# Performance work log

Measured on AMD Instinct MI355X. Metric: run time of the kernel, lower is better.

## Reference

```python
import jax, jax.numpy as jnp
import numpy as np

D_MODEL = 1024
NHEAD = 16
D_K = D_MODEL // NHEAD
THETA_NC = 0.01
B, S = 2, 2048

def setup_inputs() -> dict:
    key = jax.random.key(0)
    ks = jax.random.split(key, 8)
    lim = 1.0 / np.sqrt(D_MODEL)
    return {
        "x": jax.random.normal(ks[0], (B, S, D_MODEL), dtype=jnp.float32),
        "Wq": jax.random.uniform(ks[1], (D_MODEL, D_MODEL), jnp.float32, -lim, lim),
        "Wk": jax.random.uniform(ks[2], (D_MODEL, D_MODEL), jnp.float32, -lim, lim),
        "Wv": jax.random.uniform(ks[3], (D_MODEL, D_MODEL), jnp.float32, -lim, lim),
        "Wo": jax.random.uniform(ks[4], (D_MODEL, D_MODEL), jnp.float32, -lim, lim),
        "bo": jnp.zeros((D_MODEL,), jnp.float32),
        "gauge_phase": jnp.zeros((NHEAD,), jnp.float32),
        "gauge_amplitude": jnp.ones((NHEAD,), jnp.float32),
        "nc_mixing": jax.random.normal(ks[5], (NHEAD, D_K, D_K), jnp.float32) * THETA_NC,
    }

def reference(x, Wq, Wk, Wv, Wo, bo, gauge_phase, gauge_amplitude, nc_mixing):
    b, s, _ = x.shape
    # QKV projections (torch Linear: x @ W.T), reshape to [b, h, s, d_k]
    def proj(W):
        return (x @ W.T).reshape(b, s, NHEAD, D_K).transpose(0, 2, 1, 3)
    Q, K, V = proj(Wq), proj(Wk), proj(Wv)
    # gauge: real part of exp(i*phase) is cos(phase); amplitude scale per head
    g = (gauge_amplitude * jnp.cos(gauge_phase)).reshape(1, NHEAD, 1, 1)
    Q_nc = jnp.einsum('bhnd,hdk->bhnk', Q * g, nc_mixing)
    K_nc = jnp.einsum('bhnd,hdk->bhnk', K * g, nc_mixing)
    scores = jnp.einsum('bhnk,bhmk->bhnm', Q_nc, K_nc) / jnp.sqrt(jnp.float32(D_K))
    attn = jax.nn.softmax(scores, axis=-1)
    ctx = jnp.einsum('bhnm,bhmd->bhnd', attn, V)
    ctx = ctx.transpose(0, 2, 1, 3).reshape(b, s, D_MODEL)
    out = ctx @ Wo.T + bo
    return out, attn
```

## Files before the change

### kernel.cpp

```cpp
#include <hip/hip_runtime.h>

typedef short bf16x8 __attribute__((ext_vector_type(8)));
typedef float f32x4 __attribute__((ext_vector_type(4)));
typedef unsigned short u16;

__device__ __forceinline__ u16 f2bf(float f) {
  union { float f; unsigned u; } v; v.f = f;
  unsigned r = v.u + 0x7fffu + ((v.u >> 16) & 1u);
  return (u16)(r >> 16);
}
__device__ __forceinline__ float bf2f(u16 s) {
  union { unsigned u; float f; } v; v.u = ((unsigned)s) << 16;
  return v.f;
}

__global__ __launch_bounds__(256) void fold_kernel(
    const float* __restrict__ Wq, const float* __restrict__ Wk,
    const float* __restrict__ phase, const float* __restrict__ amp,
    const float* __restrict__ nc,
    u16* __restrict__ WqE, u16* __restrict__ WkE) {
  __shared__ float ncS[64 * 64];
  __shared__ float WS[64 * 65];
  int bid = blockIdx.x;
  int sel = bid >> 8, h = (bid >> 4) & 15, d0 = (bid & 15) * 64;
  const float* W = sel ? Wk : Wq;
  u16* O = sel ? WkE : WqE;
  float g = amp[h] * cosf(phase[h]);
  float sc = g * (sel ? 1.0f : 0.125f * 1.44269504088896f);
  int t = threadIdx.x;
  for (int l = t; l < 4096; l += 256) ncS[l] = nc[h * 4096 + l];
  for (int l = t; l < 4096; l += 256) {
    int e = l >> 6, dd = l & 63;
    WS[e * 65 + dd] = W[(h * 64 + e) * 1024 + d0 + dd];
  }
  __syncthreads();
  int kp = t >> 2, q = t & 3;
  for (int dd = q * 16; dd < q * 16 + 16; ++dd) {
    float acc = 0.f;
#pragma unroll
    for (int e = 0; e < 64; ++e) acc += WS[e * 65 + dd] * ncS[e * 64 + kp];
    O[(h * 64 + kp) * 1024 + d0 + dd] = f2bf(acc * sc);
  }
}

__global__ __launch_bounds__(256) void cast_kernel(const float* __restrict__ src,
                                                   u16* __restrict__ dst, int n4) {
  int i = blockIdx.x * 256 + threadIdx.x;
  if (i >= n4) return;
  float4 v = ((const float4*)src)[i];
  ushort4 o;
  o.x = f2bf(v.x); o.y = f2bf(v.y); o.z = f2bf(v.z); o.w = f2bf(v.w);
  ((ushort4*)dst)[i] = o;
}

__global__ __launch_bounds__(256) void split_kernel(const float* __restrict__ src,
                                                    u16* __restrict__ hi, u16* __restrict__ lo, int n4) {
  int i = blockIdx.x * 256 + threadIdx.x;
  if (i >= n4) return;
  float4 v = ((const float4*)src)[i];
  ushort4 h, l;
  h.x = f2bf(v.x); l.x = f2bf(v.x - bf2f(h.x));
  h.y = f2bf(v.y); l.y = f2bf(v.y - bf2f(h.y));
  h.z = f2bf(v.z); l.z = f2bf(v.z - bf2f(h.z));
  h.w = f2bf(v.w); l.w = f2bf(v.w - bf2f(h.w));
  ((ushort4*)hi)[i] = h;
  ((ushort4*)lo)[i] = l;
}

#define LDA 72
__global__ __launch_bounds__(256) void proj_gemm(
    const u16* __restrict__ A, const u16* __restrict__ W0, const u16* __restrict__ W1,
    const u16* __restrict__ W2, u16* __restrict__ Qnc, u16* __restrict__ Knc,
    u16* __restrict__ Vt) {
  __shared__ u16 As[128 * LDA];
  __shared__ u16 Bs[128 * LDA];
  int z = blockIdx.z;
  const u16* Wp = (z == 0) ? W0 : ((z == 1) ? W1 : W2);
  int m0 = blockIdx.x * 128, n0 = blockIdx.y * 128;
  int t = threadIdx.x, lane = t & 63, wid = t >> 6;
  int wr = wid >> 1, wc = wid & 1;
  f32x4 acc[4][4] = {};
  for (int k0 = 0; k0 < 1024; k0 += 64) {
    __syncthreads();
#pragma unroll
    for (int it = 0; it < 4; ++it) {
      int q = it * 256 + t;
      int row = q >> 3, c8 = (q & 7) * 8;
      *(bf16x8*)&As[row * LDA + c8] = *(const bf16x8*)&A[(m0 + row) * 1024 + k0 + c8];
      *(bf16x8*)&Bs[row * LDA + c8] = *(const bf16x8*)&Wp[(n0 + row) * 1024 + k0 + c8];
    }
    __syncthreads();
    bf16x8 af[4][2], bfr[4][2];
#pragma unroll
    for (int m = 0; m < 4; ++m)
#pragma unroll
      for (int kk = 0; kk < 2; ++kk) {
        af[m][kk] = *(const bf16x8*)&As[(wr * 64 + m * 16 + (lane & 15)) * LDA + kk * 32 + (lane >> 4) * 8];
        bfr[m][kk] = *(const bf16x8*)&Bs[(wc * 64 + m * 16 + (lane & 15)) * LDA + kk * 32 + (lane >> 4) * 8];
      }
#pragma unroll
    for (int kk = 0; kk < 2; ++kk)
#pragma unroll
      for (int m = 0; m < 4; ++m)
#pragma unroll
        for (int n = 0; n < 4; ++n)
          acc[m][n] = __builtin_amdgcn_mfma_f32_16x16x32_bf16(af[m][kk], bfr[n][kk], acc[m][n], 0, 0, 0);
  }
#pragma unroll
  for (int m = 0; m < 4; ++m)
#pragma unroll
    for (int n = 0; n < 4; ++n)
#pragma unroll
      for (int rr = 0; rr < 4; ++rr) {
        int row = m0 + wr * 64 + m * 16 + (lane >> 4) * 4 + rr;
        int col = n0 + wc * 64 + n * 16 + (lane & 15);
        u16 v = f2bf(acc[m][n][rr]);
        int bh = (row >> 11) * 16 + (col >> 6);
        if (z == 2)
          Vt[bh * 131072 + (col & 63) * 2048 + (row & 2047)] = v;
        else if (z == 0)
          Qnc[bh * 131072 + (row & 2047) * 64 + (col & 63)] = v;
        else
          Knc[bh * 131072 + (row & 2047) * 64 + (col & 63)] = v;
      }
}

#define PSTRIDE 72
__global__ __launch_bounds__(512, 4) void attn_kernel(
    const u16* __restrict__ Qnc, const u16* __restrict__ Knc, const u16* __restrict__ Vt,
    u16* __restrict__ ctxh, u16* __restrict__ ctxl, float* __restrict__ attn_out) {
  __shared__ u16 Ks[4096];
  __shared__ u16 Vs[4096];
  __shared__ u16 P[8][16 * PSTRIDE];
  int t = threadIdx.x, lane = t & 63, wid = t >> 6;
  int g = lane >> 4, li = lane & 15;
  int ord = blockIdx.x;
  int lid = ((ord & 7) << 6) + (ord >> 3);
  int bh = lid >> 4;
  int i0 = (lid & 15) * 128 + wid * 16;
  const u16* Qp = Qnc + bh * 131072;
  const u16* Kp = Knc + bh * 131072;
  const u16* Vp = Vt + bh * 131072;
  u16* Pw = &P[wid][0];

  int srow = (wid << 3) + (lane >> 3);
  int scol8 = lane & 7;
  int sdst = srow * 64 + (((scol8 ^ (srow & 7)) << 3));

  bf16x8 qf0 = *(const bf16x8*)&Qp[(i0 + li) * 64 + g * 8];
  bf16x8 qf1 = *(const bf16x8*)&Qp[(i0 + li) * 64 + 32 + g * 8];

  float l[4] = {0.f, 0.f, 0.f, 0.f};
  {
    bf16x8 kreg = *(const bf16x8*)&Kp[srow * 64 + scol8 * 8];
    for (int s0 = 0; s0 < 2048; s0 += 64) {
      __syncthreads();
      *(bf16x8*)&Ks[sdst] = kreg;
      __syncthreads();
      if (s0 + 64 < 2048)
        kreg = *(const bf16x8*)&Kp[(s0 + 64 + srow) * 64 + scol8 * 8];
#pragma unroll
      for (int ct = 0; ct < 4; ++ct) {
        int jr = ct * 16 + li;
        bf16x8 kf0 = *(const bf16x8*)&Ks[jr * 64 + ((g ^ (jr & 7)) << 3)];
        bf16x8 kf1 = *(const bf16x8*)&Ks[jr * 64 + (((4 + g) ^ (jr & 7)) << 3)];
        f32x4 a = {};
        a = __builtin_amdgcn_mfma_f32_16x16x32_bf16(qf0, kf0, a, 0, 0, 0);
        a = __builtin_amdgcn_mfma_f32_16x16x32_bf16(qf1, kf1, a, 0, 0, 0);
#pragma unroll
        for (int rr = 0; rr < 4; ++rr) l[rr] += __builtin_amdgcn_exp2f(a[rr]);
      }
    }
  }
  float rinv[4];
#pragma unroll
  for (int rr = 0; rr < 4; ++rr) {
    float s = l[rr];
#pragma unroll
    for (int off = 1; off < 16; off <<= 1) s += __shfl_xor(s, off);
    rinv[rr] = 1.0f / s;
  }

  f32x4 ctx[4] = {};
  float* ao = attn_out + (size_t)bh * 4194304;
  int rrow = lane >> 4;
  int rcol = (lane & 15) * 4;
  bf16x8 k2 = *(const bf16x8*)&Kp[srow * 64 + scol8 * 8];
  bf16x8 v2 = *(const bf16x8*)&Vp[srow * 2048 + scol8 * 8];
  for (int s0 = 0; s0 < 2048; s0 += 64) {
    __syncthreads();
    *(bf16x8*)&Ks[sdst] = k2;
    *(bf16x8*)&Vs[sdst] = v2;
    __syncthreads();
    if (s0 + 64 < 2048) {
      k2 = *(const bf16x8*)&Kp[(s0 + 64 + srow) * 64 + scol8 * 8];
      v2 = *(const bf16x8*)&Vp[srow * 2048 + s0 + 64 + scol8 * 8];
    }
    f32x4 acc[4];
#pragma unroll
    for (int ct = 0; ct < 4; ++ct) {
      int jr = ct * 16 + li;
      bf16x8 kf0 = *(const bf16x8*)&Ks[jr * 64 + ((g ^ (jr & 7)) << 3)];
      bf16x8 kf1 = *(const bf16x8*)&Ks[jr * 64 + (((4 + g) ^ (jr & 7)) << 3)];
      f32x4 a = {};
      a = __builtin_amdgcn_mfma_f32_16x16x32_bf16(qf0, kf0, a, 0, 0, 0);
      a = __builtin_amdgcn_mfma_f32_16x16x32_bf16(qf1, kf1, a, 0, 0, 0);
      acc[ct] = a;
    }
#pragma unroll
    for (int ct = 0; ct < 4; ++ct)
#pragma unroll
      for (int rr = 0; rr < 4; ++rr) {
        float p = __builtin_amdgcn_exp2f(acc[ct][rr]) * rinv[rr];
        Pw[(g * 4 + rr) * PSTRIDE + ct * 16 + li] = f2bf(p);
      }
    bf16x8 pa0 = *(const bf16x8*)&Pw[li * PSTRIDE + g * 8];
    bf16x8 pa1 = *(const bf16x8*)&Pw[li * PSTRIDE + 32 + g * 8];
#pragma unroll
    for (int j = 0; j < 4; ++j) {
      int row = j * 4 + rrow;
      ushort4 pv4 = *(const ushort4*)&Pw[row * PSTRIDE + rcol];
      f32x4 o = {bf2f(pv4.x), bf2f(pv4.y), bf2f(pv4.z), bf2f(pv4.w)};
      __builtin_nontemporal_store(o, (f32x4*)&ao[(size_t)(i0 + row) * 2048 + s0 + rcol]);
    }
#pragma unroll
    for (int dt = 0; dt < 4; ++dt) {
      int d = dt * 16 + li;
      bf16x8 vf0 = *(const bf16x8*)&Vs[d * 64 + ((g ^ (d & 7)) << 3)];
      bf16x8 vf1 = *(const bf16x8*)&Vs[d * 64 + (((4 + g) ^ (d & 7)) << 3)];
      ctx[dt] = __builtin_amdgcn_mfma_f32_16x16x32_bf16(pa0, vf0, ctx[dt], 0, 0, 0);
      ctx[dt] = __builtin_amdgcn_mfma_f32_16x16x32_bf16(pa1, vf1, ctx[dt], 0, 0, 0);
    }
  }
  int b = bh >> 4, hh = bh & 15;
#pragma unroll
  for (int dt = 0; dt < 4; ++dt)
#pragma unroll
    for (int rr = 0; rr < 4; ++rr) {
      int q = i0 + g * 4 + rr;
      int idx = (b * 2048 + q) * 1024 + hh * 64 + dt * 16 + li;
      float val = ctx[dt][rr];
      u16 hi = f2bf(val);
      ctxh[idx] = hi;
      ctxl[idx] = f2bf(val - bf2f(hi));
    }
}

#define LDO 40
__global__ __launch_bounds__(256) void outproj_gemm(
    const u16* __restrict__ ch, const u16* __restrict__ cl,
    const u16* __restrict__ wh, const u16* __restrict__ wl,
    const float* __restrict__ bo, float* __restrict__ out) {
  __shared__ u16 Ah[128 * LDO], Al[128 * LDO], Bh[128 * LDO], Bl[128 * LDO];
  int m0 = blockIdx.x * 128, n0 = blockIdx.y * 128;
  int t = threadIdx.x, lane = t & 63, wid = t >> 6;
  int wr = wid >> 1, wc = wid & 1;
  f32x4 acc[4][4] = {};
  for (int k0 = 0; k0 < 1024; k0 += 32) {
    __syncthreads();
#pragma unroll
    for (int it = 0; it < 2; ++it) {
      int q = it * 256 + t;
      int row = q >> 2, c8 = (q & 3) * 8;
      *(bf16x8*)&Ah[row * LDO + c8] = *(const bf16x8*)&ch[(m0 + row) * 1024 + k0 + c8];
      *(bf16x8*)&Al[row * LDO + c8] = *(const bf16x8*)&cl[(m0 + row) * 1024 + k0 + c8];
      *(bf16x8*)&Bh[row * LDO + c8] = *(const bf16x8*)&wh[(n0 + row) * 1024 + k0 + c8];
      *(bf16x8*)&Bl[row * LDO + c8] = *(const bf16x8*)&wl[(n0 + row) * 1024 + k0 + c8];
    }
    __syncthreads();
    bf16x8 ah[4], al[4], bhf[4], blf[4];
#pragma unroll
    for (int m = 0; m < 4; ++m) {
      int ar = (wr * 64 + m * 16 + (lane & 15)) * LDO + (lane >> 4) * 8;
      int br = (wc * 64 + m * 16 + (lane & 15)) * LDO + (lane >> 4) * 8;
      ah[m] = *(const bf16x8*)&Ah[ar];
      al[m] = *(const bf16x8*)&Al[ar];
      bhf[m] = *(const bf16x8*)&Bh[br];
      blf[m] = *(const bf16x8*)&Bl[br];
    }
#pragma unroll
    for (int m = 0; m < 4; ++m)
#pragma unroll
      for (int n = 0; n < 4; ++n) {
        acc[m][n] = __builtin_amdgcn_mfma_f32_16x16x32_bf16(ah[m], bhf[n], acc[m][n], 0, 0, 0);
        acc[m][n] = __builtin_amdgcn_mfma_f32_16x16x32_bf16(ah[m], blf[n], acc[m][n], 0, 0, 0);
        acc[m][n] = __builtin_amdgcn_mfma_f32_16x16x32_bf16(al[m], bhf[n], acc[m][n], 0, 0, 0);
      }
  }
#pragma unroll
  for (int m = 0; m < 4; ++m)
#pragma unroll
    for (int n = 0; n < 4; ++n)
#pragma unroll
      for (int rr = 0; rr < 4; ++rr) {
        int row = m0 + wr * 64 + m * 16 + (lane >> 4) * 4 + rr;
        int col = n0 + wc * 64 + n * 16 + (lane & 15);
        out[row * 1024 + col] = acc[m][n][rr] + bo[col];
      }
}

extern "C" void kernel_launch(void* const* d_in, const int* in_sizes, int n_in,
                              void* d_out, int out_size, void* d_ws, size_t ws_size,
                              hipStream_t stream) {
  const float* x = (const float*)d_in[0];
  const float* Wq = (const float*)d_in[1];
  const float* Wk = (const float*)d_in[2];
  const float* Wv = (const float*)d_in[3];
  const float* Wo = (const float*)d_in[4];
  const float* bo = (const float*)d_in[5];
  const float* phase = (const float*)d_in[6];
  const float* amp = (const float*)d_in[7];
  const float* nc = (const float*)d_in[8];

  float* out0 = (float*)d_out;
  float* attn = out0 + 4194304;

  u16* x_bf = (u16*)d_ws;
  u16* Qnc = x_bf + 4194304;
  u16* Knc = Qnc + 4194304;
  u16* Vt = Knc + 4194304;
  u16* ctxh = Vt + 4194304;
  u16* ctxl = ctxh + 4194304;
  u16* WqE = ctxl + 4194304;
  u16* WkE = WqE + 1048576;
  u16* Wvb = WkE + 1048576;
  u16* Woh = Wvb + 1048576;
  u16* Wol = Woh + 1048576;

  fold_kernel<<<dim3(512), dim3(256), 0, stream>>>(Wq, Wk, phase, amp, nc, WqE, WkE);
  cast_kernel<<<dim3(4096), dim3(256), 0, stream>>>(x, x_bf, 1048576);
  cast_kernel<<<dim3(1024), dim3(256), 0, stream>>>(Wv, Wvb, 262144);
  split_kernel<<<dim3(1024), dim3(256), 0, stream>>>(Wo, Woh, Wol, 262144);
  proj_gemm<<<dim3(32, 8, 3), dim3(256), 0, stream>>>(x_bf, WqE, WkE, Wvb, Qnc, Knc, Vt);
  attn_kernel<<<dim3(512), dim3(512), 0, stream>>>(Qnc, Knc, Vt, ctxh, ctxl, attn);
  outproj_gemm<<<dim3(32, 8), dim3(256), 0, stream>>>(ctxh, ctxl, Woh, Wol, bo, out0);
}
```

Measured before the change: 263.6 us.

## Prefetch GEMM tiles into registers and drop low-part ctx split in out-projection

Both GEMMs now load the next K-tile from global memory into registers while the current tile is being consumed by MFMAs, so global loads overlap with compute. The attention kernel writes only the bf16 high part of the context, and the out-projection drops the ctx-low × W-high MFMA term, going from 3 to 2 MFMAs per product. The out-projection also uses 64-column tiles with a K-step of 64, which doubles the grid. This removes a 4M-element write and read plus a third of the out-projection math, at the cost of some accuracy in the output and higher register pressure.

```diff
diff --git a/kernel.cpp b/kernel.cpp
--- a/kernel.cpp
+++ b/kernel.cpp
@@ -80,31 +80,47 @@
   int t = threadIdx.x, lane = t & 63, wid = t >> 6;
   int wr = wid >> 1, wc = wid & 1;
   f32x4 acc[4][4] = {};
+  bf16x8 pa[4], pb[4];
+#pragma unroll
+  for (int it = 0; it < 4; ++it) {
+    int q = it * 256 + t;
+    int row = q >> 3, c8 = (q & 7) * 8;
+    pa[it] = *(const bf16x8*)&A[(m0 + row) * 1024 + c8];
+    pb[it] = *(const bf16x8*)&Wp[(n0 + row) * 1024 + c8];
+  }
   for (int k0 = 0; k0 < 1024; k0 += 64) {
     __syncthreads();
 #pragma unroll
     for (int it = 0; it < 4; ++it) {
       int q = it * 256 + t;
       int row = q >> 3, c8 = (q & 7) * 8;
-      *(bf16x8*)&As[row * LDA + c8] = *(const bf16x8*)&A[(m0 + row) * 1024 + k0 + c8];
-      *(bf16x8*)&Bs[row * LDA + c8] = *(const bf16x8*)&Wp[(n0 + row) * 1024 + k0 + c8];
-    }
-    __syncthreads();
-    bf16x8 af[4][2], bfr[4][2];
-#pragma unroll
-    for (int m = 0; m < 4; ++m)
-#pragma unroll
-      for (int kk = 0; kk < 2; ++kk) {
-        af[m][kk] = *(const bf16x8*)&As[(wr * 64 + m * 16 + (lane & 15)) * LDA + kk * 32 + (lane >> 4) * 8];
-        bfr[m][kk] = *(const bf16x8*)&Bs[(wc * 64 + m * 16 + (lane & 15)) * LDA + kk * 32 + (lane >> 4) * 8];
-      }
-#pragma unroll
-    for (int kk = 0; kk < 2; ++kk)
+      *(bf16x8*)&As[row * LDA + c8] = pa[it];
+      *(bf16x8*)&Bs[row * LDA + c8] = pb[it];
+    }
+    __syncthreads();
+    if (k0 + 64 < 1024) {
+#pragma unroll
+      for (int it = 0; it < 4; ++it) {
+        int q = it * 256 + t;
+        int row = q >> 3, c8 = (q & 7) * 8;
+        pa[it] = *(const bf16x8*)&A[(m0 + row) * 1024 + k0 + 64 + c8];
+        pb[it] = *(const bf16x8*)&Wp[(n0 + row) * 1024 + k0 + 64 + c8];
+      }
+    }
+#pragma unroll
+    for (int kk = 0; kk < 2; ++kk) {
+      bf16x8 af2[4], bfr2[4];
+#pragma unroll
+      for (int m = 0; m < 4; ++m) {
+        af2[m] = *(const bf16x8*)&As[(wr * 64 + m * 16 + (lane & 15)) * LDA + kk * 32 + (lane >> 4) * 8];
+        bfr2[m] = *(const bf16x8*)&Bs[(wc * 64 + m * 16 + (lane & 15)) * LDA + kk * 32 + (lane >> 4) * 8];
+      }
 #pragma unroll
       for (int m = 0; m < 4; ++m)
 #pragma unroll
         for (int n = 0; n < 4; ++n)
-          acc[m][n] = __builtin_amdgcn_mfma_f32_16x16x32_bf16(af[m][kk], bfr[n][kk], acc[m][n], 0, 0, 0);
+          acc[m][n] = __builtin_amdgcn_mfma_f32_16x16x32_bf16(af2[m], bfr2[n], acc[m][n], 0, 0, 0);
+    }
   }
 #pragma unroll
   for (int m = 0; m < 4; ++m)
@@ -128,7 +144,7 @@
 #define PSTRIDE 72
 __global__ __launch_bounds__(512, 4) void attn_kernel(
     const u16* __restrict__ Qnc, const u16* __restrict__ Knc, const u16* __restrict__ Vt,
-    u16* __restrict__ ctxh, u16* __restrict__ ctxl, float* __restrict__ attn_out) {
+    u16* __restrict__ ctxh, float* __restrict__ attn_out) {
   __shared__ u16 Ks[4096];
   __shared__ u16 Vs[4096];
   __shared__ u16 P[8][16 * PSTRIDE];
@@ -239,62 +255,93 @@
     for (int rr = 0; rr < 4; ++rr) {
       int q = i0 + g * 4 + rr;
       int idx = (b * 2048 + q) * 1024 + hh * 64 + dt * 16 + li;
-      float val = ctx[dt][rr];
-      u16 hi = f2bf(val);
-      ctxh[idx] = hi;
-      ctxl[idx] = f2bf(val - bf2f(hi));
-    }
-}
-
-#define LDO 40
+      ctxh[idx] = f2bf(ctx[dt][rr]);
+    }
+}
+
+#define LDO 72
 __global__ __launch_bounds__(256) void outproj_gemm(
-    const u16* __restrict__ ch, const u16* __restrict__ cl,
-    const u16* __restrict__ wh, const u16* __restrict__ wl,
+    const u16* __restrict__ ch, const u16* __restrict__ wh, const u16* __restrict__ wl,
     const float* __restrict__ bo, float* __restrict__ out) {
-  __shared__ u16 Ah[128 * LDO], Al[128 * LDO], Bh[128 * LDO], Bl[128 * LDO];
-  int m0 = blockIdx.x * 128, n0 = blockIdx.y * 128;
+  __shared__ u16 Ah[128 * LDO], Bh[64 * LDO], Bl[64 * LDO];
+  int m0 = blockIdx.x * 128, n0 = blockIdx.y * 64;
   int t = threadIdx.x, lane = t & 63, wid = t >> 6;
   int wr = wid >> 1, wc = wid & 1;
-  f32x4 acc[4][4] = {};
-  for (int k0 = 0; k0 < 1024; k0 += 32) {
-    __syncthreads();
+  f32x4 acc[4][2] = {};
+  bf16x8 pa[4], pbh[2], pbl[2];
+#pragma unroll
+  for (int it = 0; it < 4; ++it) {
+    int q = it * 256 + t;
+    int row = q >> 3, c8 = (q & 7) * 8;
+    pa[it] = *(const bf16x8*)&ch[(m0 + row) * 1024 + c8];
+  }
+#pragma unroll
+  for (int it = 0; it < 2; ++it) {
+    int q = it * 256 + t;
+    int row = q >> 3, c8 = (q & 7) * 8;
+    pbh[it] = *(const bf16x8*)&wh[(n0 + row) * 1024 + c8];
+    pbl[it] = *(const bf16x8*)&wl[(n0 + row) * 1024 + c8];
+  }
+  for (int k0 = 0; k0 < 1024; k0 += 64) {
+    __syncthreads();
+#pragma unroll
+    for (int it = 0; it < 4; ++it) {
+      int q = it * 256 + t;
+      int row = q >> 3, c8 = (q & 7) * 8;
+      *(bf16x8*)&Ah[row * LDO + c8] = pa[it];
+    }
 #pragma unroll
     for (int it = 0; it < 2; ++it) {
       int q = it * 256 + t;
-      int row = q >> 2, c8 = (q & 3) * 8;
-      *(bf16x8*)&Ah[row * LDO + c8] = *(const bf16x8*)&ch[(m0 + row) * 1024 + k0 + c8];
-      *(bf16x8*)&Al[row * LDO + c8] = *(const bf16x8*)&cl[(m0 + row) * 1024 + k0 + c8];
-      *(bf16x8*)&Bh[row * LDO + c8] = *(const bf16x8*)&wh[(n0 + row) * 1024 + k0 + c8];
-      *(bf16x8*)&Bl[row * LDO + c8] = *(const bf16x8*)&wl[(n0 + row) * 1024 + k0 + c8];
-    }
-    __syncthreads();
-    bf16x8 ah[4], al[4], bhf[4], blf[4];
-#pragma unroll
-    for (int m = 0; m < 4; ++m) {
-      int ar = (wr * 64 + m * 16 + (lane & 15)) * LDO + (lane >> 4) * 8;
-      int br = (wc * 64 + m * 16 + (lane & 15)) * LDO + (lane >> 4) * 8;
-      ah[m] = *(const bf16x8*)&Ah[ar];
-      al[m] = *(const bf16x8*)&Al[ar];
-      bhf[m] = *(const bf16x8*)&Bh[br];
-      blf[m] = *(const bf16x8*)&Bl[br];
-    }
-#pragma unroll
-    for (int m = 0; m < 4; ++m)
-#pragma unroll
-      for (int n = 0; n < 4; ++n) {
-        acc[m][n] = __builtin_amdgcn_mfma_f32_16x16x32_bf16(ah[m], bhf[n], acc[m][n], 0, 0, 0);
-        acc[m][n] = __builtin_amdgcn_mfma_f32_16x16x32_bf16(ah[m], blf[n], acc[m][n], 0, 0, 0);
-        acc[m][n] = __builtin_amdgcn_mfma_f32_16x16x32_bf16(al[m], bhf[n], acc[m][n], 0, 0, 0);
-      }
+      int row = q >> 3, c8 = (q & 7) * 8;
+      *(bf16x8*)&Bh[row * LDO + c8] = pbh[it];
+      *(bf16x8*)&Bl[row * LDO + c8] = pbl[it];
+    }
+    __syncthreads();
+    if (k0 + 64 < 1024) {
+#pragma unroll
+      for (int it = 0; it < 4; ++it) {
+        int q = it * 256 + t;
+        int row = q >> 3, c8 = (q & 7) * 8;
+        pa[it] = *(const bf16x8*)&ch[(m0 + row) * 1024 + k0 + 64 + c8];
+      }
+#pragma unroll
+      for (int it = 0; it < 2; ++it) {
+        int q = it * 256 + t;
+        int row = q >> 3, c8 = (q & 7) * 8;
+        pbh[it] = *(const bf16x8*)&wh[(n0 + row) * 1024 + k0 + 64 + c8];
+        pbl[it] = *(const bf16x8*)&wl[(n0 + row) * 1024 + k0 + 64 + c8];
+      }
+    }
+#pragma unroll
+    for (int kk = 0; kk < 2; ++kk) {
+      bf16x8 ah[4], bhf[2], blf[2];
+#pragma unroll
+      for (int m = 0; m < 4; ++m)
+        ah[m] = *(const bf16x8*)&Ah[(wr * 64 + m * 16 + (lane & 15)) * LDO + kk * 32 + (lane >> 4) * 8];
+#pragma unroll
+      for (int n = 0; n < 2; ++n) {
+        int br = (wc * 32 + n * 16 + (lane & 15)) * LDO + kk * 32 + (lane >> 4) * 8;
+        bhf[n] = *(const bf16x8*)&Bh[br];
+        blf[n] = *(const bf16x8*)&Bl[br];
+      }
+#pragma unroll
+      for (int m = 0; m < 4; ++m)
+#pragma unroll
+        for (int n = 0; n < 2; ++n) {
+          acc[m][n] = __builtin_amdgcn_mfma_f32_16x16x32_bf16(ah[m], bhf[n], acc[m][n], 0, 0, 0);
+          acc[m][n] = __builtin_amdgcn_mfma_f32_16x16x32_bf16(ah[m], blf[n], acc[m][n], 0, 0, 0);
+        }
+    }
   }
 #pragma unroll
   for (int m = 0; m < 4; ++m)
 #pragma unroll
-    for (int n = 0; n < 4; ++n)
+    for (int n = 0; n < 2; ++n)
 #pragma unroll
       for (int rr = 0; rr < 4; ++rr) {
         int row = m0 + wr * 64 + m * 16 + (lane >> 4) * 4 + rr;
-        int col = n0 + wc * 64 + n * 16 + (lane & 15);
+        int col = n0 + wc * 32 + n * 16 + (lane & 15);
         out[row * 1024 + col] = acc[m][n][rr] + bo[col];
       }
 }
@@ -320,8 +367,7 @@
   u16* Knc = Qnc + 4194304;
   u16* Vt = Knc + 4194304;
   u16* ctxh = Vt + 4194304;
-  u16* ctxl = ctxh + 4194304;
-  u16* WqE = ctxl + 4194304;
+  u16* WqE = ctxh + 4194304;
   u16* WkE = WqE + 1048576;
   u16* Wvb = WkE + 1048576;
   u16* Woh = Wvb + 1048576;
@@ -332,6 +378,6 @@
   cast_kernel<<<dim3(1024), dim3(256), 0, stream>>>(Wv, Wvb, 262144);
   split_kernel<<<dim3(1024), dim3(256), 0, stream>>>(Wo, Woh, Wol, 262144);
   proj_gemm<<<dim3(32, 8, 3), dim3(256), 0, stream>>>(x_bf, WqE, WkE, Wvb, Qnc, Knc, Vt);
-  attn_kernel<<<dim3(512), dim3(512), 0, stream>>>(Qnc, Knc, Vt, ctxh, ctxl, attn);
-  outproj_gemm<<<dim3(32, 8), dim3(256), 0, stream>>>(ctxh, ctxl, Woh, Wol, bo, out0);
-}
+  attn_kernel<<<dim3(512), dim3(512), 0, stream>>>(Qnc, Knc, Vt, ctxh, attn);
+  outproj_gemm<<<dim3(32, 16), dim3(256), 0, stream>>>(ctxh, Woh, Wol, bo, out0);
+}
```

After: 234.5 us. 1.12x faster.
